# Kernel tuning notes

Hardware: AMD Instinct MI355X
Metric: run time of the kernel (lower is better)

The kernel has to match this reference:

```python
import jax, jax.numpy as jnp
import numpy as np
import math

NEG_INF = -1e30  # stand-in for float('-inf'); softmax/logsumexp treat it identically


def _fnoise(x):
    # factorized NoisyNet transform f(x) = sign(x) * sqrt(|x|)
    return jnp.sign(x) * jnp.sqrt(jnp.abs(x))


def setup_inputs() -> dict:
    B, T, D, E = 4, 4096, 2048, 16
    key = jax.random.key(0)
    ks = jax.random.split(key, 6)
    sigma_init = 0.4 / math.sqrt(D)  # sigma_zero / sqrt(in_features)
    return {
        "mh_output": jax.random.normal(ks[0], (B, T, D), dtype=jnp.float32),
        "weight": jax.random.normal(ks[1], (E, D), dtype=jnp.float32) * 0.02,
        "sigma_weight": jnp.full((E, D), sigma_init, dtype=jnp.float32),
        "bias": jax.random.normal(ks[2], (E,), dtype=jnp.float32) * 0.02,
        "sigma_bias": jnp.full((E,), sigma_init, dtype=jnp.float32),
        "eps_in": jax.random.normal(ks[3], (D,), dtype=jnp.float32),
        "eps_out": jax.random.normal(ks[4], (E,), dtype=jnp.float32),
    }


def reference(mh_output, weight, sigma_weight, bias, sigma_bias, eps_in, eps_out):
    top_k = 2
    E = weight.shape[0]

    # NoisyFactorizedLinear: W' = W + sigma_W * (f(eps_out) f(eps_in)^T)
    f_in = _fnoise(eps_in)            # [D]
    f_out = _fnoise(eps_out)          # [E]
    w_noisy = weight + sigma_weight * (f_out[:, None] * f_in[None, :])  # [E, D]
    b_noisy = bias + sigma_bias * f_out                                 # [E]
    logits = jnp.einsum("btd,ed->bte", mh_output, w_noisy) + b_noisy    # [B,T,E]
    # dropout(p=0.125) is identity in eval mode

    top_vals, indices = jax.lax.top_k(logits, top_k)                    # [B,T,k]
    # scatter top-k back into a -inf-filled tensor == mask of selected experts
    keep = jnp.sum(jax.nn.one_hot(indices, E, dtype=jnp.bool_), axis=-2)  # [B,T,E]
    sparse_logits = jnp.where(keep, logits, NEG_INF)

    router_output = jax.nn.softmax(sparse_logits, axis=-1)

    # z-loss: mean(logsumexp(sparse_logits, -1)^2); only top-k entries survive
    lse = jax.scipy.special.logsumexp(top_vals, axis=-1)                # [B,T]
    z_loss = jnp.mean(lse ** 2)

    return router_output, indices, z_loss
```

## Files before the change

### kernel.cpp

```cpp
#include <hip/hip_runtime.h>
#include <math.h>

#define NROWS 16384
#define DDIM  2048
#define NEXP  16

__device__ __forceinline__ float fnoise(float x) {
    return copysignf(sqrtf(fabsf(x)), x);
}


__global__ void prep_kernel(const float* __restrict__ weight,
                            const float* __restrict__ sigma_weight,
                            const float* __restrict__ bias,
                            const float* __restrict__ sigma_bias,
                            const float* __restrict__ eps_in,
                            const float* __restrict__ eps_out,
                            float* __restrict__ w_noisy,
                            float* __restrict__ b_noisy,
                            double* __restrict__ zacc) {
    int idx = blockIdx.x * blockDim.x + threadIdx.x;
    int e = idx >> 11;
    int d = idx & (DDIM - 1);
    float fi = fnoise(eps_in[d]);
    float fo = fnoise(eps_out[e]);
    w_noisy[idx] = weight[idx] + sigma_weight[idx] * fo * fi;
    if (idx < NEXP) {
        b_noisy[idx] = bias[idx] + sigma_bias[idx] * fnoise(eps_out[idx]);
    }
    if (idx == NEXP) { *zacc = 0.0; }
}

__global__ __launch_bounds__(256) void router_kernel(
        const float* __restrict__ x,
        const float* __restrict__ w_noisy,
        const float* __restrict__ b_noisy,
        float* __restrict__ out_router,
        float* __restrict__ out_idx,
        double* __restrict__ zacc) {
    __shared__ float wlds[NEXP * 512];
    __shared__ float zsh;

    const int tid  = threadIdx.x;
    const int wv   = tid >> 6;
    const int lane = tid & 63;
    if (tid == 0) zsh = 0.0f;

    const int rowBase = blockIdx.x * 16 + wv * 4;
    const float4* xr0 = (const float4*)(x + (size_t)(rowBase + 0) * DDIM);
    const float4* xr1 = (const float4*)(x + (size_t)(rowBase + 1) * DDIM);
    const float4* xr2 = (const float4*)(x + (size_t)(rowBase + 2) * DDIM);
    const float4* xr3 = (const float4*)(x + (size_t)(rowBase + 3) * DDIM);

    float acc[64];
    #pragma unroll
    for (int i = 0; i < 64; ++i) acc[i] = 0.0f;

    const float4* wsrc = (const float4*)w_noisy;
    float4* wdst = (float4*)wlds;

    for (int c = 0; c < 4; ++c) {
        #pragma unroll
        for (int k = 0; k < 8; ++k) {
            int f  = k * 256 + tid;
            int e  = f >> 7;
            int dj = f & 127;
            wdst[f] = wsrc[e * 512 + c * 128 + dj];
        }
        __syncthreads();

        #pragma unroll
        for (int k = 0; k < 2; ++k) {
            int p  = c * 128 + k * 64 + lane;
            int dd = k * 64 + lane;
            float4 xv0 = xr0[p];
            float4 xv1 = xr1[p];
            float4 xv2 = xr2[p];
            float4 xv3 = xr3[p];
            const float4* wrow = (const float4*)wlds;
            #pragma unroll
            for (int e = 0; e < 16; ++e) {
                float4 w = wrow[e * 128 + dd];
                float s0 = acc[0 * 16 + e];
                float s1 = acc[1 * 16 + e];
                float s2 = acc[2 * 16 + e];
                float s3 = acc[3 * 16 + e];
                s0 = fmaf(xv0.x, w.x, s0); s0 = fmaf(xv0.y, w.y, s0);
                s0 = fmaf(xv0.z, w.z, s0); s0 = fmaf(xv0.w, w.w, s0);
                s1 = fmaf(xv1.x, w.x, s1); s1 = fmaf(xv1.y, w.y, s1);
                s1 = fmaf(xv1.z, w.z, s1); s1 = fmaf(xv1.w, w.w, s1);
                s2 = fmaf(xv2.x, w.x, s2); s2 = fmaf(xv2.y, w.y, s2);
                s2 = fmaf(xv2.z, w.z, s2); s2 = fmaf(xv2.w, w.w, s2);
                s3 = fmaf(xv3.x, w.x, s3); s3 = fmaf(xv3.y, w.y, s3);
                s3 = fmaf(xv3.z, w.z, s3); s3 = fmaf(xv3.w, w.w, s3);
                acc[0 * 16 + e] = s0;
                acc[1 * 16 + e] = s1;
                acc[2 * 16 + e] = s2;
                acc[3 * 16 + e] = s3;
            }
        }
        __syncthreads();
    }

    #pragma unroll
    for (int half = 32; half >= 1; half >>= 1) {
        #pragma unroll
        for (int i = 0; i < half; ++i) {
            bool hi = (lane & half) != 0;
            float keep = hi ? acc[i + half] : acc[i];
            float send = hi ? acc[i] : acc[i + half];
            float recv = __shfl_xor(send, half, 64);
            acc[i] = keep + recv;
        }
    }

    const int e = lane & 15;
    const int r = lane >> 4;
    const int row = rowBase + r;
    float logit = acc[0] + b_noisy[e];

    float m1 = logit; int i1 = e;
    #pragma unroll
    for (int off = 8; off >= 1; off >>= 1) {
        float om = __shfl_xor(m1, off, 64);
        int   oi = __shfl_xor(i1, off, 64);
        if (om > m1 || (om == m1 && oi < i1)) { m1 = om; i1 = oi; }
    }
    float v2 = (e == i1) ? -3.4e38f : logit;
    float m2 = v2; int i2 = e;
    #pragma unroll
    for (int off = 8; off >= 1; off >>= 1) {
        float om = __shfl_xor(m2, off, 64);
        int   oi = __shfl_xor(i2, off, 64);
        if (om > m2 || (om == m2 && oi < i2)) { m2 = om; i2 = oi; }
    }

    float t = expf(m2 - m1);
    float denom = 1.0f + t;
    float p1 = 1.0f / denom;
    float val = (e == i1) ? p1 : ((e == i2) ? t * p1 : 0.0f);
    out_router[(size_t)rowBase * NEXP + lane] = val;

    if (e < 2) {
        out_idx[(size_t)row * 2 + e] = (float)((e == 0) ? i1 : i2);
    }

    if (e == 0) {
        float lse = m1 + log1pf(t);
        atomicAdd(&zsh, lse * lse);
    }
    __syncthreads();
    if (tid == 0) {
        atomicAdd(zacc, (double)zsh);
    }
}

__global__ void finalize_kernel(const double* __restrict__ zacc,
                                float* __restrict__ out) {
    if (threadIdx.x == 0 && blockIdx.x == 0) {
        out[NROWS * NEXP + NROWS * 2] = (float)(*zacc * (1.0 / (double)NROWS));
    }
}

extern "C" void kernel_launch(void* const* d_in, const int* in_sizes, int n_in,
                              void* d_out, int out_size, void* d_ws, size_t ws_size,
                              hipStream_t stream) {
    const float* mh      = (const float*)d_in[0];
    const float* weight  = (const float*)d_in[1];
    const float* sigw    = (const float*)d_in[2];
    const float* bias    = (const float*)d_in[3];
    const float* sigb    = (const float*)d_in[4];
    const float* eps_in  = (const float*)d_in[5];
    const float* eps_out = (const float*)d_in[6];

    float* out      = (float*)d_out;
    float* w_noisy  = (float*)d_ws;
    float* b_noisy  = w_noisy + NEXP * DDIM;
    double* zacc    = (double*)((char*)d_ws + NEXP * DDIM * 4 + 64);

    prep_kernel<<<(NEXP * DDIM) / 256, 256, 0, stream>>>(
        weight, sigw, bias, sigb, eps_in, eps_out, w_noisy, b_noisy, zacc);

    router_kernel<<<NROWS / 16, 256, 0, stream>>>(
        mh, w_noisy, b_noisy, out, out + NROWS * NEXP, zacc);

    finalize_kernel<<<1, 64, 0, stream>>>(zacc, out);
}
```

Baseline: 242.3 us.

## Enlarge router blocks and LDS weight chunks, replace atomic z-loss with partials

```diff
diff --git a/kernel.cpp b/kernel.cpp
--- a/kernel.cpp
+++ b/kernel.cpp
@@ -4,6 +4,8 @@
 #define NROWS 16384
 #define DDIM  2048
 #define NEXP  16
+#define RBLOCKS 512
+#define WPB 8
 
 __device__ __forceinline__ float fnoise(float x) {
     return copysignf(sqrtf(fabsf(x)), x);
@@ -17,8 +19,7 @@
                             const float* __restrict__ eps_in,
                             const float* __restrict__ eps_out,
                             float* __restrict__ w_noisy,
-                            float* __restrict__ b_noisy,
-                            double* __restrict__ zacc) {
+                            float* __restrict__ b_noisy) {
     int idx = blockIdx.x * blockDim.x + threadIdx.x;
     int e = idx >> 11;
     int d = idx & (DDIM - 1);
@@ -28,25 +29,22 @@
     if (idx < NEXP) {
         b_noisy[idx] = bias[idx] + sigma_bias[idx] * fnoise(eps_out[idx]);
     }
-    if (idx == NEXP) { *zacc = 0.0; }
 }
 
-__global__ __launch_bounds__(256) void router_kernel(
+__global__ __launch_bounds__(512, 4) void router_kernel(
         const float* __restrict__ x,
         const float* __restrict__ w_noisy,
         const float* __restrict__ b_noisy,
         float* __restrict__ out_router,
         float* __restrict__ out_idx,
-        double* __restrict__ zacc) {
-    __shared__ float wlds[NEXP * 512];
-    __shared__ float zsh;
+        float* __restrict__ zpart) {
+    __shared__ float4 wlds[NEXP * 256];
 
     const int tid  = threadIdx.x;
     const int wv   = tid >> 6;
     const int lane = tid & 63;
-    if (tid == 0) zsh = 0.0f;
 
-    const int rowBase = blockIdx.x * 16 + wv * 4;
+    const int rowBase = blockIdx.x * 32 + wv * 4;
     const float4* xr0 = (const float4*)(x + (size_t)(rowBase + 0) * DDIM);
     const float4* xr1 = (const float4*)(x + (size_t)(rowBase + 1) * DDIM);
     const float4* xr2 = (const float4*)(x + (size_t)(rowBase + 2) * DDIM);
@@ -57,30 +55,27 @@
     for (int i = 0; i < 64; ++i) acc[i] = 0.0f;
 
     const float4* wsrc = (const float4*)w_noisy;
-    float4* wdst = (float4*)wlds;
 
-    for (int c = 0; c < 4; ++c) {
+    for (int c = 0; c < 2; ++c) {
+        if (c) __syncthreads();
         #pragma unroll
-        for (int k = 0; k < 8; ++k) {
-            int f  = k * 256 + tid;
-            int e  = f >> 7;
-            int dj = f & 127;
-            wdst[f] = wsrc[e * 512 + c * 128 + dj];
+        for (int j = 0; j < 8; ++j) {
+            int f = j * 512 + tid;
+            wlds[f] = wsrc[(f >> 8) * 512 + c * 256 + (f & 255)];
         }
         __syncthreads();
 
-        #pragma unroll
-        for (int k = 0; k < 2; ++k) {
-            int p  = c * 128 + k * 64 + lane;
+        #pragma unroll 2
+        for (int k = 0; k < 4; ++k) {
+            int p  = c * 256 + k * 64 + lane;
             int dd = k * 64 + lane;
             float4 xv0 = xr0[p];
             float4 xv1 = xr1[p];
             float4 xv2 = xr2[p];
             float4 xv3 = xr3[p];
-            const float4* wrow = (const float4*)wlds;
             #pragma unroll
             for (int e = 0; e < 16; ++e) {
-                float4 w = wrow[e * 128 + dd];
+                float4 w = wlds[e * 256 + dd];
                 float s0 = acc[0 * 16 + e];
                 float s1 = acc[1 * 16 + e];
                 float s2 = acc[2 * 16 + e];
@@ -99,7 +94,6 @@
                 acc[3 * 16 + e] = s3;
             }
         }
-        __syncthreads();
     }
 
     #pragma unroll
@@ -136,8 +130,7 @@
     }
 
     float t = expf(m2 - m1);
-    float denom = 1.0f + t;
-    float p1 = 1.0f / denom;
+    float p1 = 1.0f / (1.0f + t);
     float val = (e == i1) ? p1 : ((e == i2) ? t * p1 : 0.0f);
     out_router[(size_t)rowBase * NEXP + lane] = val;
 
@@ -145,20 +138,31 @@
         out_idx[(size_t)row * 2 + e] = (float)((e == 0) ? i1 : i2);
     }
 
+    float zv = 0.0f;
     if (e == 0) {
         float lse = m1 + log1pf(t);
-        atomicAdd(&zsh, lse * lse);
+        zv = lse * lse;
     }
-    __syncthreads();
-    if (tid == 0) {
-        atomicAdd(zacc, (double)zsh);
+    zv += __shfl_xor(zv, 16, 64);
+    zv += __shfl_xor(zv, 32, 64);
+    if (lane == 0) {
+        zpart[blockIdx.x * WPB + wv] = zv;
     }
 }
 
-__global__ void finalize_kernel(const double* __restrict__ zacc,
+__global__ void finalize_kernel(const float* __restrict__ zpart,
                                 float* __restrict__ out) {
-    if (threadIdx.x == 0 && blockIdx.x == 0) {
-        out[NROWS * NEXP + NROWS * 2] = (float)(*zacc * (1.0 / (double)NROWS));
+    __shared__ float ws4[4];
+    int tid = threadIdx.x;
+    float s = 0.0f;
+    for (int i = tid; i < RBLOCKS * WPB; i += 256) s += zpart[i];
+    #pragma unroll
+    for (int off = 32; off >= 1; off >>= 1) s += __shfl_xor(s, off, 64);
+    if ((tid & 63) == 0) ws4[tid >> 6] = s;
+    __syncthreads();
+    if (tid == 0) {
+        float total = ws4[0] + ws4[1] + ws4[2] + ws4[3];
+        out[NROWS * NEXP + NROWS * 2] = total * (1.0f / (float)NROWS);
     }
 }
 
@@ -176,13 +180,13 @@
     float* out      = (float*)d_out;
     float* w_noisy  = (float*)d_ws;
     float* b_noisy  = w_noisy + NEXP * DDIM;
-    double* zacc    = (double*)((char*)d_ws + NEXP * DDIM * 4 + 64);
+    float* zpart    = w_noisy + 32800;
 
     prep_kernel<<<(NEXP * DDIM) / 256, 256, 0, stream>>>(
-        weight, sigw, bias, sigb, eps_in, eps_out, w_noisy, b_noisy, zacc);
+        weight, sigw, bias, sigb, eps_in, eps_out, w_noisy, b_noisy);
 
-    router_kernel<<<NROWS / 16, 256, 0, stream>>>(
-        mh, w_noisy, b_noisy, out, out + NROWS * NEXP, zacc);
+    router_kernel<<<RBLOCKS, 512, 0, stream>>>(
+        mh, w_noisy, b_noisy, out, out + NROWS * NEXP, zpart);
 
-    finalize_kernel<<<1, 64, 0, stream>>>(zacc, out);
+    finalize_kernel<<<1, 256, 0, stream>>>(zpart, out);
 }
```

New measurement: 215.5 us. 1.12x faster.
